# Optimization experiments

Hardware: AMD Instinct MI355X
Metric: run time of the kernel (lower is better)

The kernel has to match this reference:

```python
import jax, jax.numpy as jnp
import numpy as np

DIM = 512
HEADS = 8
BLOCKS = 6
DFF = 2048
B = 4
T = 2048
VOCAB = 20
CLASSES = 1
MAX_TOKENS = 5000
EPS = 1e-5


def _make_pe():
    # Sinusoidal positional encoding, identical to PositionalEncodingSin
    pos = np.arange(MAX_TOKENS, dtype=np.float32)[:, None]
    div = np.exp(np.arange(0, DIM, 2, dtype=np.float32) * (-np.log(10000.0) / DIM))
    pe = np.zeros((MAX_TOKENS, DIM), dtype=np.float32)
    pe[:, 0::2] = np.sin(pos * div)
    pe[:, 1::2] = np.cos(pos * div)
    return jnp.asarray(pe)


def setup_inputs() -> dict:
    key = jax.random.key(0)
    ks = jax.random.split(key, 8)

    def n(k, shape, s=0.02):
        return (jax.random.normal(k, shape) * s).astype(jnp.float32)

    x = jax.random.randint(ks[0], (B, T), 0, VOCAB, dtype=jnp.int32)
    embed = n(ks[1], (VOCAB, DIM))
    pe = _make_pe()
    Wqkv = n(ks[2], (BLOCKS, DIM, 3 * DIM))   # to_qvk (no bias)
    W0 = n(ks[3], (BLOCKS, DIM, DIM))          # W_0 (no bias)
    g1 = jnp.ones((BLOCKS, DIM), jnp.float32)
    b1 = jnp.zeros((BLOCKS, DIM), jnp.float32)
    g2 = jnp.ones((BLOCKS, DIM), jnp.float32)
    b2 = jnp.zeros((BLOCKS, DIM), jnp.float32)
    Wl1 = n(ks[4], (BLOCKS, DIM, DFF))
    bl1 = jnp.zeros((BLOCKS, DFF), jnp.float32)
    Wl2 = n(ks[5], (BLOCKS, DFF, DIM))
    bl2 = jnp.zeros((BLOCKS, DIM), jnp.float32)
    Whead = n(ks[6], (DIM, CLASSES))
    bhead = jnp.zeros((CLASSES,), jnp.float32)
    return dict(x=x, embed=embed, pe=pe, Wqkv=Wqkv, W0=W0, g1=g1, b1=b1,
                g2=g2, b2=b2, Wl1=Wl1, bl1=bl1, Wl2=Wl2, bl2=bl2,
                Whead=Whead, bhead=bhead)


def _ln(x, g, b):
    mu = x.mean(-1, keepdims=True)
    var = ((x - mu) ** 2).mean(-1, keepdims=True)
    return (x - mu) / jnp.sqrt(var + EPS) * g + b


def _mhsa(x, Wqkv, W0):
    b, t, _ = x.shape
    dh = DIM // HEADS
    qkv = x @ Wqkv                                   # [b, t, 3*DIM]
    # rearrange 'b t (d k h) -> k b h t d' with k=3, h=HEADS
    qkv = qkv.reshape(b, t, dh, 3, HEADS).transpose(3, 0, 4, 1, 2)
    q, k, v = qkv[0], qkv[1], qkv[2]                 # [b, h, t, dh]
    scores = jnp.einsum('bhid,bhjd->bhij', q, k) * (dh ** -0.5)
    attn = jax.nn.softmax(scores, axis=-1)
    out = jnp.einsum('bhij,bhjd->bhid', attn, v)
    out = out.transpose(0, 2, 1, 3).reshape(b, t, DIM)  # 'b h t d -> b t (h d)'
    return out @ W0


def _forward(x, embed, pe, Wqkv, W0, g1, b1, g2, b2, Wl1, bl1, Wl2, bl2, Whead, bhead):
    h = embed[x] + pe[None, :x.shape[1], :]          # embedding + sinusoidal PE (dropout off)
    for i in range(BLOCKS):                          # post-norm transformer blocks
        a = _mhsa(h, Wqkv[i], W0[i])
        y = _ln(a + h, g1[i], b1[i])
        m = jax.nn.gelu(y @ Wl1[i] + bl1[i], approximate=False) @ Wl2[i] + bl2[i]
        h = _ln(m + y, g2[i], b2[i])
    return (h @ Whead + bhead).squeeze(-1)           # [B, T]


def reference(x, embed, pe, Wqkv, W0, g1, b1, g2, b2, Wl1, bl1, Wl2, bl2, Whead, bhead):
    return _forward(x, embed, pe, Wqkv, W0, g1, b1, g2, b2, Wl1, bl1, Wl2, bl2, Whead, bhead)
```

## Files before the change

kernel.cpp:

```cpp
#include <hip/hip_runtime.h>
#include <hip/hip_bf16.h>
#include <math.h>

#define DIMD 512
#define HEADS 8
#define NBLK 6
#define DFF 2048
#define BATCH 4
#define SEQ 2048
#define NTOK 8192
#define DH 64
#define LNEPS 1e-5f
#define QSCALE 0.1803368801111204f

typedef __bf16 bf16;
typedef __bf16 bf16x8 __attribute__((ext_vector_type(8)));
typedef __bf16 bf16x4 __attribute__((ext_vector_type(4)));
typedef float f32x4 __attribute__((ext_vector_type(4)));
typedef float f32x16 __attribute__((ext_vector_type(16)));

__device__ __forceinline__ void async16(const void* g, void* l) {
  __builtin_amdgcn_global_load_lds(
      (const __attribute__((address_space(1))) void*)g,
      (__attribute__((address_space(3))) void*)l, 16, 0, 0);
}

__device__ __forceinline__ int swz(int r) { return ((r >> 1) ^ (r >> 3)) & 3; }

__global__ void k_cvt_t(const float* __restrict__ in, bf16* __restrict__ out, int K, int N) {
  __shared__ float T[32][33];
  const float* src = in + (size_t)blockIdx.z * K * N;
  bf16* dst = out + (size_t)blockIdx.z * K * N;
  int k0 = blockIdx.y * 32, n0 = blockIdx.x * 32;
  int r = threadIdx.x >> 3, c4 = (threadIdx.x & 7) * 4;
  float4 v = *reinterpret_cast<const float4*>(src + (size_t)(k0 + r) * N + n0 + c4);
  T[r][c4] = v.x; T[r][c4 + 1] = v.y; T[r][c4 + 2] = v.z; T[r][c4 + 3] = v.w;
  __syncthreads();
  bf16x4 o;
  o[0] = (bf16)T[c4][r]; o[1] = (bf16)T[c4 + 1][r];
  o[2] = (bf16)T[c4 + 2][r]; o[3] = (bf16)T[c4 + 3][r];
  *reinterpret_cast<bf16x4*>(dst + (size_t)(n0 + r) * K + k0 + c4) = o;
}

__global__ void k_cvt_qkv(const float* __restrict__ in, bf16* __restrict__ out, int K, int N) {
  __shared__ float T[32][33];
  const float* src = in + (size_t)blockIdx.z * K * N;
  bf16* dst = out + (size_t)blockIdx.z * K * N;
  int k0 = blockIdx.y * 32, n0 = blockIdx.x * 32;
  int r = threadIdx.x >> 3, c4 = (threadIdx.x & 7) * 4;
  float4 v = *reinterpret_cast<const float4*>(src + (size_t)(k0 + r) * N + n0 + c4);
  T[r][c4] = v.x; T[r][c4 + 1] = v.y; T[r][c4 + 2] = v.z; T[r][c4 + 3] = v.w;
  __syncthreads();
  int n_src = n0 + r;
  int d = n_src / 24;
  int rem = n_src - d * 24;
  int np = (rem >> 3) * 512 + (rem & 7) * 64 + d;
  bf16x4 o;
  o[0] = (bf16)T[c4][r]; o[1] = (bf16)T[c4 + 1][r];
  o[2] = (bf16)T[c4 + 2][r]; o[3] = (bf16)T[c4 + 3][r];
  *reinterpret_cast<bf16x4*>(dst + (size_t)np * K + k0 + c4) = o;
}

__global__ void k_embed(const int* __restrict__ x, const float* __restrict__ embed,
                        const float* __restrict__ pe, bf16* __restrict__ hb,
                        float* __restrict__ hf) {
  int row = blockIdx.x;
  int t = row & (SEQ - 1);
  int tok = x[row];
  int c = threadIdx.x * 2;
  const float* e = embed + (size_t)tok * DIMD;
  const float* p = pe + (size_t)t * DIMD;
  float v0 = e[c] + p[c];
  float v1 = e[c + 1] + p[c + 1];
  size_t o = (size_t)row * DIMD + c;
  hb[o] = (bf16)v0; hb[o + 1] = (bf16)v1;
  hf[o] = v0;       hf[o + 1] = v1;
}

enum { EPI_QKV = 0, EPI_RES = 1, EPI_GELU = 2, EPI_BIASRES = 3 };

template <int EPI, int MT>
__global__ __launch_bounds__(256) void k_gemm(
    const bf16* __restrict__ A, const bf16* __restrict__ Wt,
    const float* __restrict__ bias, const float* __restrict__ resf,
    bf16* __restrict__ out0, bf16* __restrict__ out1, bf16* __restrict__ out2,
    float* __restrict__ outf, int N, int K) {
  constexpr int TJ = (MT == 128) ? 2 : 1;
  __shared__ bf16 As[MT][32];
  __shared__ bf16 Bs[128][32];
  int tid = threadIdx.x;
  int w = tid >> 6, lane = tid & 63, hi = lane >> 5, l31 = lane & 31;
  int m0 = blockIdx.y * MT, n0 = blockIdx.x * 128;
  int wr = (MT == 128) ? (w >> 1) : 0;
  int wc = (MT == 128) ? (w & 1) : w;

  const bf16 *Ag0, *Ag1 = nullptr, *Bg0, *Bg1;
  bf16 *dA0, *dA1 = nullptr, *dB0, *dB1;
  if (MT == 128) {
    int ra0 = w * 32 + (lane >> 2), ra1 = ra0 + 16;
    Ag0 = A + (size_t)(m0 + ra0) * K + ((lane & 3) ^ swz(ra0)) * 8;
    Ag1 = A + (size_t)(m0 + ra1) * K + ((lane & 3) ^ swz(ra1)) * 8;
    Bg0 = Wt + (size_t)(n0 + ra0) * K + ((lane & 3) ^ swz(ra0)) * 8;
    Bg1 = Wt + (size_t)(n0 + ra1) * K + ((lane & 3) ^ swz(ra1)) * 8;
    dA0 = &As[0][0] + w * 1024; dA1 = dA0 + 512;
    dB0 = &Bs[0][0] + w * 1024; dB1 = dB0 + 512;
  } else {
    int ra = w * 16 + (lane >> 2);
    Ag0 = A + (size_t)(m0 + ra) * K + ((lane & 3) ^ swz(ra)) * 8;
    int rb0 = w * 16 + (lane >> 2), rb1 = rb0 + 64;
    Bg0 = Wt + (size_t)(n0 + rb0) * K + ((lane & 3) ^ swz(rb0)) * 8;
    Bg1 = Wt + (size_t)(n0 + rb1) * K + ((lane & 3) ^ swz(rb1)) * 8;
    dA0 = &As[0][0] + w * 512;
    dB0 = &Bs[0][0] + w * 512; dB1 = dB0 + 2048;
  }

  int rowA[2], fA[2], colB[2], fB[2];
#pragma unroll
  for (int i = 0; i < 2; ++i) {
    rowA[i] = ((MT == 128) ? wr * 64 : 0) + i * 32 + l31;
    fA[i] = swz(rowA[i]);
  }
#pragma unroll
  for (int j = 0; j < TJ; ++j) {
    colB[j] = ((MT == 128) ? (wc * 64 + j * 32) : (wc * 32)) + l31;
    fB[j] = swz(colB[j]);
  }

  f32x16 acc[2][TJ] = {};

  for (int k0 = 0; k0 < K; k0 += 32) {
    async16(Ag0 + k0, dA0);
    if (MT == 128) async16(Ag1 + k0, dA1);
    async16(Bg0 + k0, dB0);
    async16(Bg1 + k0, dB1);
    __syncthreads();

#pragma unroll
    for (int s = 0; s < 2; ++s) {
      int lc = s * 2 + hi;
      bf16x8 af[2], bfr[TJ];
#pragma unroll
      for (int i = 0; i < 2; ++i)
        af[i] = *reinterpret_cast<const bf16x8*>(&As[rowA[i]][(lc ^ fA[i]) * 8]);
#pragma unroll
      for (int j = 0; j < TJ; ++j)
        bfr[j] = *reinterpret_cast<const bf16x8*>(&Bs[colB[j]][(lc ^ fB[j]) * 8]);
#pragma unroll
      for (int i = 0; i < 2; ++i)
#pragma unroll
        for (int j = 0; j < TJ; ++j)
          acc[i][j] = __builtin_amdgcn_mfma_f32_32x32x16_bf16(af[i], bfr[j], acc[i][j], 0, 0, 0);
    }
    __syncthreads();
  }

#pragma unroll
  for (int j = 0; j < TJ; ++j) {
    int col = n0 + ((MT == 128) ? (wc * 64 + j * 32) : (wc * 32)) + l31;
    int qwhich = 0, qhh = 0, qdd = 0;
    float bcol = 0.f;
    if (EPI == EPI_QKV) {
      qwhich = col >> 9; qhh = (col >> 6) & 7; qdd = col & 63;
    } else if (EPI == EPI_GELU || EPI == EPI_BIASRES) {
      bcol = bias[col];
    }
#pragma unroll
    for (int i = 0; i < 2; ++i) {
#pragma unroll
      for (int reg = 0; reg < 16; ++reg) {
        int row = m0 + ((MT == 128) ? wr * 64 : 0) + i * 32 + (reg & 3) + 8 * (reg >> 2) + 4 * hi;
        float v = acc[i][j][reg];
        if (EPI == EPI_QKV) {
          int b = row >> 11;
          int t = row & (SEQ - 1);
          int bh = b * HEADS + qhh;
          if (qwhich == 0)      out0[((size_t)bh * SEQ + t) * DH + qdd] = (bf16)(v * QSCALE);
          else if (qwhich == 1) out1[((size_t)bh * SEQ + t) * DH + qdd] = (bf16)v;
          else                  out2[((size_t)bh * DH + qdd) * SEQ + t] = (bf16)v;
        } else if (EPI == EPI_RES) {
          outf[(size_t)row * N + col] = v + resf[(size_t)row * N + col];
        } else if (EPI == EPI_GELU) {
          float xv = v + bcol;
          out0[(size_t)row * N + col] = (bf16)(0.5f * xv * (1.0f + erff(xv * 0.70710678118f)));
        } else {
          outf[(size_t)row * N + col] = v + bcol + resf[(size_t)row * N + col];
        }
      }
    }
  }
}

__global__ __launch_bounds__(256) void k_attn(const bf16* __restrict__ q,
                                              const bf16* __restrict__ k,
                                              const bf16* __restrict__ vt,
                                              bf16* __restrict__ out) {
  __shared__ bf16 Ks[64][64];
  __shared__ bf16 Vs[64][64];
  __shared__ bf16 Pw[4][2][16][72];
  int tid = threadIdx.x;
  int w = tid >> 6, lane = tid & 63, quad = lane >> 4, l15 = lane & 15;
  int qt = blockIdx.x, bh = blockIdx.y;
  const bf16* qbase = q + (size_t)bh * SEQ * DH;
  const bf16* kbase = k + (size_t)bh * SEQ * DH;
  const bf16* vbase = vt + (size_t)bh * DH * SEQ;

  bf16x8 qf[2][2];
#pragma unroll
  for (int s = 0; s < 2; ++s) {
    int qrow = qt * 128 + s * 64 + w * 16 + l15;
    qf[s][0] = *reinterpret_cast<const bf16x8*>(qbase + (size_t)qrow * DH + quad * 8);
    qf[s][1] = *reinterpret_cast<const bf16x8*>(qbase + (size_t)qrow * DH + 32 + quad * 8);
  }

  int strow = w * 16 + (lane >> 3);
  int scol = ((lane & 7) ^ (lane >> 3)) * 8;
  const bf16* kp = kbase + (size_t)strow * DH + scol;
  const bf16* vp = vbase + (size_t)strow * SEQ + scol;
  bf16* kdst = &Ks[0][0] + (size_t)w * 1024 + (size_t)lane * 8;
  bf16* vdst = &Vs[0][0] + (size_t)w * 1024 + (size_t)lane * 8;

  f32x4 Ot[2][4] = {};
  float ls[2] = {0.f, 0.f};
  int fx = (l15 & 7);

  bf16x8 ka = *reinterpret_cast<const bf16x8*>(kp);
  bf16x8 kb = *reinterpret_cast<const bf16x8*>(kp + (size_t)8 * DH);
  bf16x8 va = *reinterpret_cast<const bf16x8*>(vp);
  bf16x8 vb = *reinterpret_cast<const bf16x8*>(vp + (size_t)8 * SEQ);
  kp += (size_t)64 * DH;

  for (int j0 = 0; j0 < SEQ; j0 += 64) {
    __syncthreads();
    *reinterpret_cast<bf16x8*>(kdst) = ka;
    *reinterpret_cast<bf16x8*>(kdst + 512) = kb;
    *reinterpret_cast<bf16x8*>(vdst) = va;
    *reinterpret_cast<bf16x8*>(vdst + 512) = vb;
    __syncthreads();
    if (j0 + 64 < SEQ) {
      ka = *reinterpret_cast<const bf16x8*>(kp);
      kb = *reinterpret_cast<const bf16x8*>(kp + (size_t)8 * DH);
      va = *reinterpret_cast<const bf16x8*>(vp + j0 + 64);
      vb = *reinterpret_cast<const bf16x8*>(vp + j0 + 64 + (size_t)8 * SEQ);
      kp += (size_t)64 * DH;
    }

    f32x4 st[2][4];
#pragma unroll
    for (int nt = 0; nt < 4; ++nt) {
      bf16x8 kf0 = *reinterpret_cast<const bf16x8*>(&Ks[nt * 16 + l15][(quad ^ fx) * 8]);
      bf16x8 kf1 = *reinterpret_cast<const bf16x8*>(&Ks[nt * 16 + l15][((quad + 4) ^ fx) * 8]);
#pragma unroll
      for (int s = 0; s < 2; ++s) {
        f32x4 z = {};
        z = __builtin_amdgcn_mfma_f32_16x16x32_bf16(kf0, qf[s][0], z, 0, 0, 0);
        z = __builtin_amdgcn_mfma_f32_16x16x32_bf16(kf1, qf[s][1], z, 0, 0, 0);
        st[s][nt] = z;
      }
    }

#pragma unroll
    for (int s = 0; s < 2; ++s)
#pragma unroll
      for (int nt = 0; nt < 4; ++nt) {
#pragma unroll
        for (int r = 0; r < 4; ++r) {
          float p = exp2f(st[s][nt][r]);
          st[s][nt][r] = p;
          ls[s] += p;
        }
        bf16x4 pv;
        pv[0] = (bf16)st[s][nt][0]; pv[1] = (bf16)st[s][nt][1];
        pv[2] = (bf16)st[s][nt][2]; pv[3] = (bf16)st[s][nt][3];
        *reinterpret_cast<bf16x4*>(&Pw[w][s][l15][nt * 16 + quad * 4]) = pv;
      }

#pragma unroll
    for (int h = 0; h < 2; ++h) {
      bf16x8 pf0 = *reinterpret_cast<const bf16x8*>(&Pw[w][0][l15][h * 32 + quad * 8]);
      bf16x8 pf1 = *reinterpret_cast<const bf16x8*>(&Pw[w][1][l15][h * 32 + quad * 8]);
#pragma unroll
      for (int nt = 0; nt < 4; ++nt) {
        bf16x8 vf = *reinterpret_cast<const bf16x8*>(&Vs[nt * 16 + l15][((quad + 4 * h) ^ fx) * 8]);
        Ot[0][nt] = __builtin_amdgcn_mfma_f32_16x16x32_bf16(vf, pf0, Ot[0][nt], 0, 0, 0);
        Ot[1][nt] = __builtin_amdgcn_mfma_f32_16x16x32_bf16(vf, pf1, Ot[1][nt], 0, 0, 0);
      }
    }
  }

  int b = bh >> 3, hh = bh & 7;
  int qr = lane >> 2, c0 = (lane & 3) * 16;
#pragma unroll
  for (int s = 0; s < 2; ++s) {
    float l = ls[s];
    l += __shfl_xor(l, 16);
    l += __shfl_xor(l, 32);
    float inv = 1.0f / l;
#pragma unroll
    for (int nt = 0; nt < 4; ++nt) {
      bf16x4 ov;
      ov[0] = (bf16)(Ot[s][nt][0] * inv); ov[1] = (bf16)(Ot[s][nt][1] * inv);
      ov[2] = (bf16)(Ot[s][nt][2] * inv); ov[3] = (bf16)(Ot[s][nt][3] * inv);
      *reinterpret_cast<bf16x4*>(&Pw[w][s][l15][nt * 16 + quad * 4]) = ov;
    }
    bf16x8 o0 = *reinterpret_cast<const bf16x8*>(&Pw[w][s][qr][c0]);
    bf16x8 o1 = *reinterpret_cast<const bf16x8*>(&Pw[w][s][qr][c0 + 8]);
    int token = b * SEQ + qt * 128 + s * 64 + w * 16 + qr;
    *reinterpret_cast<bf16x8*>(out + (size_t)token * DIMD + hh * DH + c0) = o0;
    *reinterpret_cast<bf16x8*>(out + (size_t)token * DIMD + hh * DH + c0 + 8) = o1;
  }
}

__global__ void k_ln(const float* __restrict__ in, const float* __restrict__ g,
                     const float* __restrict__ b, bf16* __restrict__ outb,
                     float* __restrict__ outf) {
  int wid = (blockIdx.x * blockDim.x + threadIdx.x) >> 6;
  int lane = threadIdx.x & 63;
  const float* row = in + (size_t)wid * DIMD;
  float4 x0 = *reinterpret_cast<const float4*>(row + lane * 8);
  float4 x1 = *reinterpret_cast<const float4*>(row + lane * 8 + 4);
  float xs[8] = {x0.x, x0.y, x0.z, x0.w, x1.x, x1.y, x1.z, x1.w};
  float s = 0.f, sq = 0.f;
#pragma unroll
  for (int j = 0; j < 8; ++j) { s += xs[j]; sq += xs[j] * xs[j]; }
#pragma unroll
  for (int m = 1; m < 64; m <<= 1) { s += __shfl_xor(s, m); sq += __shfl_xor(sq, m); }
  float mu = s * (1.0f / DIMD);
  float var = sq * (1.0f / DIMD) - mu * mu;
  float rstd = rsqrtf(var + LNEPS);
  bf16x8 ov;
#pragma unroll
  for (int j = 0; j < 8; ++j) {
    int c = lane * 8 + j;
    float y = (xs[j] - mu) * rstd * g[c] + b[c];
    ov[j] = (bf16)y;
    outf[(size_t)wid * DIMD + c] = y;
  }
  *reinterpret_cast<bf16x8*>(outb + (size_t)wid * DIMD + lane * 8) = ov;
}

__global__ void k_head(const bf16* __restrict__ h, const float* __restrict__ w,
                       const float* __restrict__ bh, float* __restrict__ out) {
  int row = (blockIdx.x * blockDim.x + threadIdx.x) >> 6;
  int lane = threadIdx.x & 63;
  bf16x8 xv = *reinterpret_cast<const bf16x8*>(h + (size_t)row * DIMD + lane * 8);
  float s = 0.f;
#pragma unroll
  for (int j = 0; j < 8; ++j) s += (float)xv[j] * w[lane * 8 + j];
#pragma unroll
  for (int m = 1; m < 64; m <<= 1) s += __shfl_xor(s, m);
  if (lane == 0) out[row] = s + bh[0];
}

extern "C" void kernel_launch(void* const* d_in, const int* in_sizes, int n_in,
                              void* d_out, int out_size, void* d_ws, size_t ws_size,
                              hipStream_t stream) {
  const int*   x     = (const int*)d_in[0];
  const float* embed = (const float*)d_in[1];
  const float* pe    = (const float*)d_in[2];
  const float* Wqkv  = (const float*)d_in[3];
  const float* W0    = (const float*)d_in[4];
  const float* g1    = (const float*)d_in[5];
  const float* b1    = (const float*)d_in[6];
  const float* g2    = (const float*)d_in[7];
  const float* b2    = (const float*)d_in[8];
  const float* Wl1   = (const float*)d_in[9];
  const float* bl1   = (const float*)d_in[10];
  const float* Wl2   = (const float*)d_in[11];
  const float* bl2   = (const float*)d_in[12];
  const float* Whead = (const float*)d_in[13];
  const float* bhead = (const float*)d_in[14];
  float* outp = (float*)d_out;

  char* ws = (char*)d_ws;
  size_t off = 0;
  auto alloc = [&](size_t bytes) { void* p = ws + off; off += (bytes + 255) & ~(size_t)255; return p; };
  const size_t ACT = (size_t)NTOK * DIMD;
  bf16*  hb   = (bf16*)alloc(ACT * 2);
  float* hf   = (float*)alloc(ACT * 4);
  bf16*  qb   = (bf16*)alloc(ACT * 2);
  bf16*  kb   = (bf16*)alloc(ACT * 2);
  bf16*  vtb  = (bf16*)alloc(ACT * 2);
  bf16*  ao   = (bf16*)alloc(ACT * 2);
  float* r32  = (float*)alloc(ACT * 4);
  bf16*  yb   = (bf16*)alloc(ACT * 2);
  float* yf   = (float*)alloc(ACT * 4);
  bf16*  wqkt = (bf16*)alloc((size_t)NBLK * DIMD * 3 * DIMD * 2);
  bf16*  w0t  = (bf16*)alloc((size_t)NBLK * DIMD * DIMD * 2);
  bf16*  wl1t = (bf16*)alloc((size_t)NBLK * DIMD * DFF * 2);
  bf16*  wl2t = (bf16*)alloc((size_t)NBLK * DFF * DIMD * 2);
  bf16*  mid  = qb;

  k_cvt_qkv<<<dim3(3 * DIMD / 32, DIMD / 32, NBLK), 256, 0, stream>>>(Wqkv, wqkt, DIMD, 3 * DIMD);
  k_cvt_t<<<dim3(DIMD / 32, DIMD / 32, NBLK), 256, 0, stream>>>(W0, w0t, DIMD, DIMD);
  k_cvt_t<<<dim3(DFF / 32, DIMD / 32, NBLK), 256, 0, stream>>>(Wl1, wl1t, DIMD, DFF);
  k_cvt_t<<<dim3(DIMD / 32, DFF / 32, NBLK), 256, 0, stream>>>(Wl2, wl2t, DFF, DIMD);

  k_embed<<<NTOK, 256, 0, stream>>>(x, embed, pe, hb, hf);
  for (int i = 0; i < NBLK; ++i) {
    k_gemm<EPI_QKV, 128><<<dim3(3 * DIMD / 128, NTOK / 128), 256, 0, stream>>>(
        hb, wqkt + (size_t)i * DIMD * 3 * DIMD, nullptr, nullptr,
        qb, kb, vtb, nullptr, 3 * DIMD, DIMD);
    k_attn<<<dim3(SEQ / 128, BATCH * HEADS), 256, 0, stream>>>(qb, kb, vtb, ao);
    k_gemm<EPI_RES, 64><<<dim3(DIMD / 128, NTOK / 64), 256, 0, stream>>>(
        ao, w0t + (size_t)i * DIMD * DIMD, nullptr, hf,
        nullptr, nullptr, nullptr, r32, DIMD, DIMD);
    k_ln<<<NTOK / 4, 256, 0, stream>>>(r32, g1 + i * DIMD, b1 + i * DIMD, yb, yf);
    k_gemm<EPI_GELU, 128><<<dim3(DFF / 128, NTOK / 128), 256, 0, stream>>>(
        yb, wl1t + (size_t)i * DIMD * DFF, bl1 + (size_t)i * DFF, nullptr,
        mid, nullptr, nullptr, nullptr, DFF, DIMD);
    k_gemm<EPI_BIASRES, 64><<<dim3(DIMD / 128, NTOK / 64), 256, 0, stream>>>(
        mid, wl2t + (size_t)i * DFF * DIMD, bl2 + (size_t)i * DIMD, yf,
        nullptr, nullptr, nullptr, r32, DIMD, DFF);
    k_ln<<<NTOK / 4, 256, 0, stream>>>(r32, g2 + i * DIMD, b2 + i * DIMD, hb, hf);
  }
  k_head<<<NTOK / 4, 256, 0, stream>>>(hb, Whead, bhead, outp);
}
```

Before: 1.390 ms.

## Double-buffer GEMM LDS tiles, deepen attention K/V prefetch, remap attention blocks to XCDs

```diff
diff --git a/kernel.cpp b/kernel.cpp
--- a/kernel.cpp
+++ b/kernel.cpp
@@ -86,8 +86,8 @@
     bf16* __restrict__ out0, bf16* __restrict__ out1, bf16* __restrict__ out2,
     float* __restrict__ outf, int N, int K) {
   constexpr int TJ = (MT == 128) ? 2 : 1;
-  __shared__ bf16 As[MT][32];
-  __shared__ bf16 Bs[128][32];
+  __shared__ bf16 As[2][MT][32];
+  __shared__ bf16 Bs[2][128][32];
   int tid = threadIdx.x;
   int w = tid >> 6, lane = tid & 63, hi = lane >> 5, l31 = lane & 31;
   int m0 = blockIdx.y * MT, n0 = blockIdx.x * 128;
@@ -95,23 +95,23 @@
   int wc = (MT == 128) ? (w & 1) : w;
 
   const bf16 *Ag0, *Ag1 = nullptr, *Bg0, *Bg1;
-  bf16 *dA0, *dA1 = nullptr, *dB0, *dB1;
+  int dA0, dA1 = 0, dB0, dB1;
   if (MT == 128) {
     int ra0 = w * 32 + (lane >> 2), ra1 = ra0 + 16;
     Ag0 = A + (size_t)(m0 + ra0) * K + ((lane & 3) ^ swz(ra0)) * 8;
     Ag1 = A + (size_t)(m0 + ra1) * K + ((lane & 3) ^ swz(ra1)) * 8;
     Bg0 = Wt + (size_t)(n0 + ra0) * K + ((lane & 3) ^ swz(ra0)) * 8;
     Bg1 = Wt + (size_t)(n0 + ra1) * K + ((lane & 3) ^ swz(ra1)) * 8;
-    dA0 = &As[0][0] + w * 1024; dA1 = dA0 + 512;
-    dB0 = &Bs[0][0] + w * 1024; dB1 = dB0 + 512;
+    dA0 = w * 1024; dA1 = dA0 + 512;
+    dB0 = w * 1024; dB1 = dB0 + 512;
   } else {
     int ra = w * 16 + (lane >> 2);
     Ag0 = A + (size_t)(m0 + ra) * K + ((lane & 3) ^ swz(ra)) * 8;
-    int rb0 = w * 16 + (lane >> 2), rb1 = rb0 + 64;
-    Bg0 = Wt + (size_t)(n0 + rb0) * K + ((lane & 3) ^ swz(rb0)) * 8;
+    int rb1 = ra + 64;
+    Bg0 = Wt + (size_t)(n0 + ra) * K + ((lane & 3) ^ swz(ra)) * 8;
     Bg1 = Wt + (size_t)(n0 + rb1) * K + ((lane & 3) ^ swz(rb1)) * 8;
-    dA0 = &As[0][0] + w * 512;
-    dB0 = &Bs[0][0] + w * 512; dB1 = dB0 + 2048;
+    dA0 = w * 512;
+    dB0 = w * 512; dB1 = dB0 + 2048;
   }
 
   int rowA[2], fA[2], colB[2], fB[2];
@@ -128,30 +128,39 @@
 
   f32x16 acc[2][TJ] = {};
 
-  for (int k0 = 0; k0 < K; k0 += 32) {
-    async16(Ag0 + k0, dA0);
-    if (MT == 128) async16(Ag1 + k0, dA1);
-    async16(Bg0 + k0, dB0);
-    async16(Bg1 + k0, dB1);
+  auto stage = [&](int it) {
+    int buf = it & 1;
+    bf16* a = &As[buf][0][0];
+    bf16* b = &Bs[buf][0][0];
+    int k0 = it * 32;
+    async16(Ag0 + k0, a + dA0);
+    if (MT == 128) async16(Ag1 + k0, a + dA1);
+    async16(Bg0 + k0, b + dB0);
+    async16(Bg1 + k0, b + dB1);
+  };
+
+  int nit = K / 32;
+  stage(0);
+  for (int it = 0; it < nit; ++it) {
+    int buf = it & 1;
     __syncthreads();
-
+    if (it + 1 < nit) stage(it + 1);
 #pragma unroll
     for (int s = 0; s < 2; ++s) {
       int lc = s * 2 + hi;
       bf16x8 af[2], bfr[TJ];
 #pragma unroll
       for (int i = 0; i < 2; ++i)
-        af[i] = *reinterpret_cast<const bf16x8*>(&As[rowA[i]][(lc ^ fA[i]) * 8]);
+        af[i] = *reinterpret_cast<const bf16x8*>(&As[buf][rowA[i]][(lc ^ fA[i]) * 8]);
 #pragma unroll
       for (int j = 0; j < TJ; ++j)
-        bfr[j] = *reinterpret_cast<const bf16x8*>(&Bs[colB[j]][(lc ^ fB[j]) * 8]);
+        bfr[j] = *reinterpret_cast<const bf16x8*>(&Bs[buf][colB[j]][(lc ^ fB[j]) * 8]);
 #pragma unroll
       for (int i = 0; i < 2; ++i)
 #pragma unroll
         for (int j = 0; j < TJ; ++j)
           acc[i][j] = __builtin_amdgcn_mfma_f32_32x32x16_bf16(af[i], bfr[j], acc[i][j], 0, 0, 0);
     }
-    __syncthreads();
   }
 
 #pragma unroll
@@ -199,7 +208,10 @@
   __shared__ bf16 Pw[4][2][16][72];
   int tid = threadIdx.x;
   int w = tid >> 6, lane = tid & 63, quad = lane >> 4, l15 = lane & 15;
-  int qt = blockIdx.x, bh = blockIdx.y;
+  int f = blockIdx.y * gridDim.x + blockIdx.x;
+  int xcd = f & 7, g = f >> 3;
+  int bh = xcd * 4 + (g >> 4);
+  int qt = g & 15;
   const bf16* qbase = q + (size_t)bh * SEQ * DH;
   const bf16* kbase = k + (size_t)bh * SEQ * DH;
   const bf16* vbase = vt + (size_t)bh * DH * SEQ;
@@ -223,25 +235,30 @@
   float ls[2] = {0.f, 0.f};
   int fx = (l15 & 7);
 
-  bf16x8 ka = *reinterpret_cast<const bf16x8*>(kp);
-  bf16x8 kb = *reinterpret_cast<const bf16x8*>(kp + (size_t)8 * DH);
-  bf16x8 va = *reinterpret_cast<const bf16x8*>(vp);
-  bf16x8 vb = *reinterpret_cast<const bf16x8*>(vp + (size_t)8 * SEQ);
-  kp += (size_t)64 * DH;
-
-  for (int j0 = 0; j0 < SEQ; j0 += 64) {
+  bf16x8 pre_k[2][2], pre_v[2][2];
+#pragma unroll
+  for (int t = 0; t < 2; ++t) {
+    pre_k[t][0] = *reinterpret_cast<const bf16x8*>(kp + (size_t)t * 64 * DH);
+    pre_k[t][1] = *reinterpret_cast<const bf16x8*>(kp + (size_t)t * 64 * DH + 8 * DH);
+    pre_v[t][0] = *reinterpret_cast<const bf16x8*>(vp + t * 64);
+    pre_v[t][1] = *reinterpret_cast<const bf16x8*>(vp + t * 64 + (size_t)8 * SEQ);
+  }
+
+  const int nit = SEQ / 64;
+  for (int it = 0; it < nit; ++it) {
+    int cur = it & 1;
     __syncthreads();
-    *reinterpret_cast<bf16x8*>(kdst) = ka;
-    *reinterpret_cast<bf16x8*>(kdst + 512) = kb;
-    *reinterpret_cast<bf16x8*>(vdst) = va;
-    *reinterpret_cast<bf16x8*>(vdst + 512) = vb;
+    *reinterpret_cast<bf16x8*>(kdst) = pre_k[cur][0];
+    *reinterpret_cast<bf16x8*>(kdst + 512) = pre_k[cur][1];
+    *reinterpret_cast<bf16x8*>(vdst) = pre_v[cur][0];
+    *reinterpret_cast<bf16x8*>(vdst + 512) = pre_v[cur][1];
     __syncthreads();
-    if (j0 + 64 < SEQ) {
-      ka = *reinterpret_cast<const bf16x8*>(kp);
-      kb = *reinterpret_cast<const bf16x8*>(kp + (size_t)8 * DH);
-      va = *reinterpret_cast<const bf16x8*>(vp + j0 + 64);
-      vb = *reinterpret_cast<const bf16x8*>(vp + j0 + 64 + (size_t)8 * SEQ);
-      kp += (size_t)64 * DH;
+    if (it + 2 < nit) {
+      size_t ko = (size_t)(it + 2) * 64;
+      pre_k[cur][0] = *reinterpret_cast<const bf16x8*>(kp + ko * DH);
+      pre_k[cur][1] = *reinterpret_cast<const bf16x8*>(kp + ko * DH + 8 * DH);
+      pre_v[cur][0] = *reinterpret_cast<const bf16x8*>(vp + ko);
+      pre_v[cur][1] = *reinterpret_cast<const bf16x8*>(vp + ko + (size_t)8 * SEQ);
     }
 
     f32x4 st[2][4];
```

New measurement: 3.370 ms. 2.42x slower.
